# Kernel optimization log

Measured on AMD Instinct MI355X. Metric: run time of the kernel, lower is better.

The kernel has to match this reference:

```python
import jax, jax.numpy as jnp
import numpy as np

C_IN = 192
HEADS = 6
QKV_DIM = C_IN // HEADS  # 32
WH = WW = 4              # window_size
PAD_H = WH // 2          # 2
PAD_W = WW // 2          # 2


def setup_inputs() -> dict:
    key = jax.random.key(0)
    ks = jax.random.split(key, 6)
    s = 0.02
    return {
        "x": jax.random.normal(ks[0], (8, C_IN, 128, 128), jnp.float32),
        "w_qkv1": jax.random.normal(ks[1], (3 * C_IN, C_IN), jnp.float32) * s,
        "b_qkv1": jnp.zeros((3 * C_IN,), jnp.float32),
        "w_qkv2": jax.random.normal(ks[2], (3 * C_IN, C_IN), jnp.float32) * s,
        "b_qkv2": jnp.zeros((3 * C_IN,), jnp.float32),
        "w_head": jax.random.normal(ks[3], (C_IN, 2 * C_IN), jnp.float32) * s,  # 1x1 conv as matmul
        "b_head": jnp.zeros((C_IN,), jnp.float32),
    }


def _window_partition(x):
    # bchw_to_bnc: [B,C,H,W] -> [B*nh*nw, WH*WW, C]
    B, C, H, W = x.shape
    nh, nw = H // WH, W // WW
    x = x.reshape(B, C, nh, WH, nw, WW)
    x = x.transpose(0, 2, 4, 3, 5, 1)  # B,nh,nw,WH,WW,C
    return x.reshape(B * nh * nw, WH * WW, C)


def _window_merge(x, out_shape):
    # bnc_to_bchw: inverse of _window_partition
    B, C, H, W = out_shape
    nh, nw = H // WH, W // WW
    x = x.reshape(B, nh, nw, WH, WW, C)
    x = x.transpose(0, 5, 1, 3, 2, 4)  # B,C,nh,WH,nw,WW
    return x.reshape(B, C, H, W)


def _mha(xw, w, b):
    # xw: [Bn, N=16, C]; fused QKV projection then per-window SDPA
    Bn, N, C = xw.shape
    qkv = xw @ w.T + b
    q, k, v = jnp.split(qkv, 3, axis=-1)
    to_heads = lambda t: t.reshape(Bn, N, HEADS, QKV_DIM).transpose(0, 2, 1, 3)
    q, k, v = to_heads(q), to_heads(k), to_heads(v)
    scale = 1.0 / np.sqrt(QKV_DIM).astype(np.float32)
    attn = jax.nn.softmax(jnp.einsum('bhnd,bhmd->bhnm', q, k) * scale, axis=-1)
    o = jnp.einsum('bhnm,bhmd->bhnd', attn, v)
    return o.transpose(0, 2, 1, 3).reshape(Bn, N, C)


def reference(x, w_qkv1, b_qkv1, w_qkv2, b_qkv2, w_head, b_head):
    # branch 2: zero-pad by window//2 on each side (shifted windows)
    x2 = jnp.pad(x, ((0, 0), (0, 0), (PAD_H, PAD_H), (PAD_W, PAD_W)))
    s1, s2 = x.shape, x2.shape
    o1 = _window_merge(_mha(_window_partition(x), w_qkv1, b_qkv1), s1)
    o2 = _window_merge(_mha(_window_partition(x2), w_qkv2, b_qkv2), s2)
    o2 = o2[:, :, PAD_H:-PAD_H, PAD_W:-PAD_W]  # negative pad = crop
    o = jnp.concatenate([o1, o2], axis=1)      # [B, 2C, H, W]
    # 1x1 conv head projection
    return jnp.einsum('bchw,oc->bohw', o, w_head) + b_head[None, :, None, None]
```

## Files before the change

### kernel.cpp

```cpp
#include <hip/hip_runtime.h>


typedef unsigned short u16;
using bf16x8 = __attribute__((ext_vector_type(8))) short;
using f32x4  = __attribute__((ext_vector_type(4))) float;
using u16x8  = __attribute__((ext_vector_type(8))) unsigned short;
using u16x4  = __attribute__((ext_vector_type(4))) unsigned short;

#define CIN   192
#define CQKV  576
#define NW2   33

__device__ __forceinline__ float bf2f(u16 u) {
    unsigned int x = ((unsigned int)u) << 16;
    float f; __builtin_memcpy(&f, &x, 4); return f;
}
__device__ __forceinline__ u16 f2bf(float f) {
    unsigned int x; __builtin_memcpy(&x, &f, 4);
    return (u16)((x + 0x7FFFu + ((x >> 16) & 1u)) >> 16);
}
__device__ __forceinline__ int xcol(int c, int tok) {
    int blk = (c >> 3) ^ ((tok ^ (tok >> 4)) & 7);
    return blk * 8 + (c & 7);
}

__global__ void prep_conv(const float* __restrict__ w1, const float* __restrict__ w2,
                          const float* __restrict__ wh,
                          u16* __restrict__ w1b, u16* __restrict__ w2b, u16* __restrict__ whb) {
    int i = blockIdx.x * 256 + threadIdx.x;
    if (i < 110592)        w1b[i] = f2bf(w1[i]);
    else if (i < 221184)   w2b[i - 110592] = f2bf(w2[i - 110592]);
    else                   whb[i - 221184] = f2bf(wh[i - 221184]);
}

template<int BR>
__global__ __launch_bounds__(256, 2) void qkv_attn(const float* __restrict__ x,
                                                   const u16* __restrict__ wb,
                                                   const float* __restrict__ bias,
                                                   u16* __restrict__ ocat) {
    __shared__ __align__(16) char smem[77824];
    u16* xl = (u16*)smem;
    u16* wl = (u16*)(smem + 25600);
    u16* qk = (u16*)smem;
    u16* vt = (u16*)(smem + 50176);
    u16* pl = (u16*)(smem + 74752);

    const int tid  = threadIdx.x;
    const int wave = tid >> 6, lane = tid & 63;
    const int lo16 = lane & 15, quad = lane >> 4;

    int b, wy, g;
    if (BR == 0) {
        int bi = blockIdx.x;
        b = bi >> 8; int rem = bi & 255;
        wy = rem >> 3; g = rem & 7;
    } else {
        int bi = blockIdx.x;
        b = bi / 297; int rem = bi % 297;
        wy = rem / 9; g = rem % 9;
    }
    const int hbase = wy * 4, wbase = g * 16;

#pragma unroll
    for (int it = 0; it < 12; ++it) {
        int i = it * 256 + tid;
        int c = i >> 4, y = (i >> 2) & 3, xc = i & 3;
        float e0, e1, e2, e3;
        if (BR == 0) {
            const float4 v = *reinterpret_cast<const float4*>(
                &x[(((size_t)b * CIN + c) * 128 + hbase + y) * 128 + wbase + xc * 4]);
            e0 = v.x; e1 = v.y; e2 = v.z; e3 = v.w;
        } else {
            int h = hbase + y - 2;
            int w0 = wbase + xc * 4 - 2;
            bool hok = (unsigned)h < 128u;
            const float* row = &x[(((size_t)b * CIN + c) * 128 + h) * 128];
            if (hok && w0 >= 0 && w0 + 3 < 128) {
                float2 p0 = *reinterpret_cast<const float2*>(&row[w0]);
                float2 p1 = *reinterpret_cast<const float2*>(&row[w0 + 2]);
                e0 = p0.x; e1 = p0.y; e2 = p1.x; e3 = p1.y;
            } else {
                e0 = (hok && w0 >= 0 && w0 < 128)         ? row[w0]     : 0.f;
                e1 = (hok && w0+1 >= 0 && w0+1 < 128)     ? row[w0 + 1] : 0.f;
                e2 = (hok && w0+2 >= 0 && w0+2 < 128)     ? row[w0 + 2] : 0.f;
                e3 = (hok && w0+3 >= 0 && w0+3 < 128)     ? row[w0 + 3] : 0.f;
            }
        }
        int t0 = xc * 16 + y * 4;
        xl[(t0 + 0) * 200 + xcol(c, t0 + 0)] = f2bf(e0);
        xl[(t0 + 1) * 200 + xcol(c, t0 + 1)] = f2bf(e1);
        xl[(t0 + 2) * 200 + xcol(c, t0 + 2)] = f2bf(e2);
        xl[(t0 + 3) * 200 + xcol(c, t0 + 3)] = f2bf(e3);
    }
    __syncthreads();

    f32x4 acc[9][4];
#pragma unroll
    for (int mt = 0; mt < 9; ++mt)
#pragma unroll
        for (int nt = 0; nt < 4; ++nt) acc[mt][nt] = f32x4{0.f, 0.f, 0.f, 0.f};

    for (int s = 0; s < 6; ++s) {
#pragma unroll
        for (int it = 0; it < 9; ++it) {
            int i = it * 256 + tid;
            int co = i >> 2, kk = (i & 3) * 8;
            u16x8 v = *reinterpret_cast<const u16x8*>(&wb[co * 192 + s * 32 + kk]);
            *reinterpret_cast<u16x8*>(&wl[co * 40 + kk]) = v;
        }
        __syncthreads();
        bf16x8 bfr[4];
#pragma unroll
        for (int nt = 0; nt < 4; ++nt) {
            int tok = nt * 16 + lo16;
            int kb = s * 4 + quad;
            bfr[nt] = *reinterpret_cast<const bf16x8*>(
                &xl[tok * 200 + (((kb ^ ((tok ^ (tok >> 4)) & 7)) << 3))]);
        }
#pragma unroll
        for (int mt = 0; mt < 9; ++mt) {
            bf16x8 afr = *reinterpret_cast<const bf16x8*>(
                &wl[(wave * 144 + mt * 16 + lo16) * 40 + quad * 8]);
#pragma unroll
            for (int nt = 0; nt < 4; ++nt)
                acc[mt][nt] = __builtin_amdgcn_mfma_f32_16x16x32_bf16(afr, bfr[nt], acc[mt][nt], 0, 0, 0);
        }
        __syncthreads();
    }

    const float scale = 0.17677669529663687f;
#pragma unroll
    for (int mt = 0; mt < 9; ++mt) {
        int co0 = wave * 144 + mt * 16 + quad * 4;
        const float4 bv = *reinterpret_cast<const float4*>(&bias[co0]);
#pragma unroll
        for (int nt = 0; nt < 4; ++nt) {
            int tok = nt * 16 + lo16;
            float v0 = acc[mt][nt][0] + bv.x, v1 = acc[mt][nt][1] + bv.y;
            float v2 = acc[mt][nt][2] + bv.z, v3 = acc[mt][nt][3] + bv.w;
            if (co0 < 192) { v0 *= scale; v1 *= scale; v2 *= scale; v3 *= scale; }
            if (co0 < 384) {
                u16x4 pk = {f2bf(v0), f2bf(v1), f2bf(v2), f2bf(v3)};
                *reinterpret_cast<u16x4*>(&qk[tok * 392 + co0]) = pk;
            } else {
                int dh = co0 - 384;
                int head = dh >> 5, d0 = dh & 31;
                int win = tok >> 4, m = tok & 15;
                u16* vrow = &vt[((win * 6 + head) * 32 + d0) * 16 + m];
                vrow[0]  = f2bf(v0);
                vrow[16] = f2bf(v1);
                vrow[32] = f2bf(v2);
                vrow[48] = f2bf(v3);
            }
        }
    }
    __syncthreads();

    {
        const int win = wave;
        const u16* qbase = qk + (size_t)(win * 16) * 392;
        const bf16x8 z8 = {};
        const f32x4 zc = {0.f, 0.f, 0.f, 0.f};
        bool dov; size_t dst = 0;
        if (BR == 0) {
            int wg = wy * 32 + g * 4 + win;
            dst = (((size_t)(b * 1024 + wg)) * 16 + lo16) * 384;
            dov = true;
        } else {
            int wx = g * 4 + win;
            int h = wy * 4 + (lo16 >> 2) - 2;
            int w = wx * 4 + (lo16 & 3) - 2;
            dov = (wx < NW2) && (unsigned)h < 128u && (unsigned)w < 128u;
            if (dov) {
                int wg = (h >> 2) * 32 + (w >> 2);
                int nn = (h & 3) * 4 + (w & 3);
                dst = (((size_t)(b * 1024 + wg)) * 16 + nn) * 384 + 192;
            }
        }
#pragma unroll
        for (int head = 0; head < 6; ++head) {
            bf16x8 kfr = *reinterpret_cast<const bf16x8*>(
                &qbase[lo16 * 392 + 192 + head * 32 + quad * 8]);
            bf16x8 qfr = *reinterpret_cast<const bf16x8*>(
                &qbase[lo16 * 392 + head * 32 + quad * 8]);
            f32x4 st = __builtin_amdgcn_mfma_f32_16x16x32_bf16(kfr, qfr, zc, 0, 0, 0);
            float mx = fmaxf(fmaxf(st[0], st[1]), fmaxf(st[2], st[3]));
            mx = fmaxf(mx, __shfl_xor(mx, 16));
            mx = fmaxf(mx, __shfl_xor(mx, 32));
            float p0 = __expf(st[0] - mx), p1 = __expf(st[1] - mx);
            float p2 = __expf(st[2] - mx), p3 = __expf(st[3] - mx);
            float sum = p0 + p1 + p2 + p3;
            sum += __shfl_xor(sum, 16);
            sum += __shfl_xor(sum, 32);
            float inv = 1.0f / sum;
            u16x4 pk = {f2bf(p0), f2bf(p1), f2bf(p2), f2bf(p3)};
            *reinterpret_cast<u16x4*>(&pl[(wave * 16 + lo16) * 24 + quad * 4]) = pk;
            bf16x8 pf = (quad < 2)
                ? *reinterpret_cast<const bf16x8*>(&pl[(wave * 16 + lo16) * 24 + quad * 8]) : z8;
            const u16* vbase = &vt[(win * 6 + head) * 32 * 16];
#pragma unroll
            for (int half = 0; half < 2; ++half) {
                bf16x8 av = (quad < 2)
                    ? *reinterpret_cast<const bf16x8*>(&vbase[(half * 16 + lo16) * 16 + quad * 8]) : z8;
                f32x4 o = __builtin_amdgcn_mfma_f32_16x16x32_bf16(av, pf, zc, 0, 0, 0);
                if (dov) {
                    u16x4 ok = {f2bf(o[0] * inv), f2bf(o[1] * inv),
                                f2bf(o[2] * inv), f2bf(o[3] * inv)};
                    *reinterpret_cast<u16x4*>(&ocat[dst + head * 32 + half * 16 + quad * 4]) = ok;
                }
            }
        }
    }
}

__global__ __launch_bounds__(256, 3) void head_gemm(const u16* __restrict__ ocat,
                                                    const u16* __restrict__ whb,
                                                    const float* __restrict__ bh,
                                                    float* __restrict__ out) {
    __shared__ __align__(16) u16 bt[64 * 392];
    const int tid = threadIdx.x;
    const int wave = tid >> 6, lane = tid & 63;
    const int lo16 = lane & 15, quad = lane >> 4;

    int bi = blockIdx.x;
    int b = bi >> 8; int rem = bi & 255;
    int wy = rem >> 3, g = rem & 7;
    const int wg0 = wy * 32 + g * 4;
    const size_t gbase = ((size_t)(b * 1024 + wg0) * 16) * 384;

#pragma unroll
    for (int it = 0; it < 12; ++it) {
        int i = it * 256 + tid;
        u16x8 v = *reinterpret_cast<const u16x8*>(&ocat[gbase + (size_t)i * 8]);
        int row = i / 48, kc = i - row * 48;
        *reinterpret_cast<u16x8*>(&bt[row * 392 + kc * 8]) = v;
    }
    __syncthreads();

    const int co_base = wave * 48;
    f32x4 acc[3][4];
#pragma unroll
    for (int mt = 0; mt < 3; ++mt)
#pragma unroll
        for (int nt = 0; nt < 4; ++nt) acc[mt][nt] = f32x4{0.f, 0.f, 0.f, 0.f};

#pragma unroll
    for (int s = 0; s < 12; ++s) {
        int k0 = s * 32;
        bf16x8 a[3], bb[4];
#pragma unroll
        for (int nt = 0; nt < 4; ++nt)
            bb[nt] = *reinterpret_cast<const bf16x8*>(&bt[(nt * 16 + lo16) * 392 + k0 + quad * 8]);
#pragma unroll
        for (int mt = 0; mt < 3; ++mt)
            a[mt] = *reinterpret_cast<const bf16x8*>(
                &whb[(size_t)(co_base + mt * 16 + lo16) * 384 + k0 + quad * 8]);
#pragma unroll
        for (int mt = 0; mt < 3; ++mt)
#pragma unroll
            for (int nt = 0; nt < 4; ++nt)
                acc[mt][nt] = __builtin_amdgcn_mfma_f32_16x16x32_bf16(a[mt], bb[nt], acc[mt][nt], 0, 0, 0);
    }

    int h = wy * 4 + (lo16 >> 2);
#pragma unroll
    for (int mt = 0; mt < 3; ++mt) {
        int co0 = co_base + mt * 16 + quad * 4;
        const float4 bv = *reinterpret_cast<const float4*>(&bh[co0]);
#pragma unroll
        for (int r = 0; r < 4; ++r) {
            float bias = (r == 0) ? bv.x : (r == 1) ? bv.y : (r == 2) ? bv.z : bv.w;
#pragma unroll
            for (int nt = 0; nt < 4; ++nt) {
                int w = (g * 4 + nt) * 4 + (lo16 & 3);
                out[(((size_t)b * CIN + co0 + r) * 128 + h) * 128 + w] = acc[mt][nt][r] + bias;
            }
        }
    }
}

extern "C" void kernel_launch(void* const* d_in, const int* in_sizes, int n_in,
                              void* d_out, int out_size, void* d_ws, size_t ws_size,
                              hipStream_t stream) {
    const float* x  = (const float*)d_in[0];
    const float* w1 = (const float*)d_in[1];
    const float* b1 = (const float*)d_in[2];
    const float* w2 = (const float*)d_in[3];
    const float* b2 = (const float*)d_in[4];
    const float* wh = (const float*)d_in[5];
    const float* bh = (const float*)d_in[6];
    float* out = (float*)d_out;

    char* ws = (char*)d_ws;
    u16* ocat = (u16*)ws;
    u16* w1b  = (u16*)(ws + 100663296);
    u16* w2b  = (u16*)(ws + 100884480);
    u16* whb  = (u16*)(ws + 101105664);

    prep_conv<<<1152, 256, 0, stream>>>(w1, w2, wh, w1b, w2b, whb);
    qkv_attn<0><<<2048, 256, 0, stream>>>(x, w1b, b1, ocat);
    qkv_attn<1><<<2376, 256, 0, stream>>>(x, w2b, b2, ocat);
    head_gemm<<<2048, 256, 0, stream>>>(ocat, whb, bh, out);
}
```

Baseline: 455.5 us.

## Merge both attention branches into one launch and read weights straight from global

The two templated branch kernels become a single launch of 4424 blocks. A swizzled block index interleaves branch-0 and branch-1 blocks across XCDs, and each block picks its weights, bias and load path at runtime. The per-K-step weight staging into LDS and its two barriers are removed; each wave now loads its A fragments directly from global or L2. This cuts barrier stalls and the kernel-launch gap, but adds uncoalesced-ish global loads in the MFMA loop, possibly higher latency, and runtime branching where the branch used to be a compile-time template.

```diff
diff --git a/kernel.cpp b/kernel.cpp
--- a/kernel.cpp
+++ b/kernel.cpp
@@ -33,14 +33,14 @@
     else                   whb[i - 221184] = f2bf(wh[i - 221184]);
 }
 
-template<int BR>
 __global__ __launch_bounds__(256, 2) void qkv_attn(const float* __restrict__ x,
-                                                   const u16* __restrict__ wb,
-                                                   const float* __restrict__ bias,
+                                                   const u16* __restrict__ w1b,
+                                                   const float* __restrict__ b1,
+                                                   const u16* __restrict__ w2b,
+                                                   const float* __restrict__ b2,
                                                    u16* __restrict__ ocat) {
     __shared__ __align__(16) char smem[77824];
     u16* xl = (u16*)smem;
-    u16* wl = (u16*)(smem + 25600);
     u16* qk = (u16*)smem;
     u16* vt = (u16*)(smem + 50176);
     u16* pl = (u16*)(smem + 74752);
@@ -49,28 +49,42 @@
     const int wave = tid >> 6, lane = tid & 63;
     const int lo16 = lane & 15, quad = lane >> 4;
 
+    const int swz = (blockIdx.x & 7) * 553 + (blockIdx.x >> 3);
+    const bool br0 = (swz < 2048);
+
     int b, wy, g;
-    if (BR == 0) {
-        int bi = blockIdx.x;
-        b = bi >> 8; int rem = bi & 255;
+    const u16* wb; const float* bias;
+    if (br0) {
+        b = swz >> 8; int rem = swz & 255;
         wy = rem >> 3; g = rem & 7;
+        wb = w1b; bias = b1;
     } else {
-        int bi = blockIdx.x;
+        int bi = swz - 2048;
         b = bi / 297; int rem = bi % 297;
         wy = rem / 9; g = rem % 9;
+        wb = w2b; bias = b2;
     }
     const int hbase = wy * 4, wbase = g * 16;
 
-#pragma unroll
-    for (int it = 0; it < 12; ++it) {
-        int i = it * 256 + tid;
-        int c = i >> 4, y = (i >> 2) & 3, xc = i & 3;
-        float e0, e1, e2, e3;
-        if (BR == 0) {
+    if (br0) {
+#pragma unroll
+        for (int it = 0; it < 12; ++it) {
+            int i = it * 256 + tid;
+            int c = i >> 4, y = (i >> 2) & 3, xc = i & 3;
             const float4 v = *reinterpret_cast<const float4*>(
                 &x[(((size_t)b * CIN + c) * 128 + hbase + y) * 128 + wbase + xc * 4]);
-            e0 = v.x; e1 = v.y; e2 = v.z; e3 = v.w;
-        } else {
+            int t0 = xc * 16 + y * 4;
+            xl[(t0 + 0) * 200 + xcol(c, t0 + 0)] = f2bf(v.x);
+            xl[(t0 + 1) * 200 + xcol(c, t0 + 1)] = f2bf(v.y);
+            xl[(t0 + 2) * 200 + xcol(c, t0 + 2)] = f2bf(v.z);
+            xl[(t0 + 3) * 200 + xcol(c, t0 + 3)] = f2bf(v.w);
+        }
+    } else {
+#pragma unroll
+        for (int it = 0; it < 12; ++it) {
+            int i = it * 256 + tid;
+            int c = i >> 4, y = (i >> 2) & 3, xc = i & 3;
+            float e0, e1, e2, e3;
             int h = hbase + y - 2;
             int w0 = wbase + xc * 4 - 2;
             bool hok = (unsigned)h < 128u;
@@ -85,12 +99,12 @@
                 e2 = (hok && w0+2 >= 0 && w0+2 < 128)     ? row[w0 + 2] : 0.f;
                 e3 = (hok && w0+3 >= 0 && w0+3 < 128)     ? row[w0 + 3] : 0.f;
             }
-        }
-        int t0 = xc * 16 + y * 4;
-        xl[(t0 + 0) * 200 + xcol(c, t0 + 0)] = f2bf(e0);
-        xl[(t0 + 1) * 200 + xcol(c, t0 + 1)] = f2bf(e1);
-        xl[(t0 + 2) * 200 + xcol(c, t0 + 2)] = f2bf(e2);
-        xl[(t0 + 3) * 200 + xcol(c, t0 + 3)] = f2bf(e3);
+            int t0 = xc * 16 + y * 4;
+            xl[(t0 + 0) * 200 + xcol(c, t0 + 0)] = f2bf(e0);
+            xl[(t0 + 1) * 200 + xcol(c, t0 + 1)] = f2bf(e1);
+            xl[(t0 + 2) * 200 + xcol(c, t0 + 2)] = f2bf(e2);
+            xl[(t0 + 3) * 200 + xcol(c, t0 + 3)] = f2bf(e3);
+        }
     }
     __syncthreads();
 
@@ -100,15 +114,9 @@
 #pragma unroll
         for (int nt = 0; nt < 4; ++nt) acc[mt][nt] = f32x4{0.f, 0.f, 0.f, 0.f};
 
+    const u16* wrow = wb + (size_t)(wave * 144 + lo16) * 192 + quad * 8;
+#pragma unroll
     for (int s = 0; s < 6; ++s) {
-#pragma unroll
-        for (int it = 0; it < 9; ++it) {
-            int i = it * 256 + tid;
-            int co = i >> 2, kk = (i & 3) * 8;
-            u16x8 v = *reinterpret_cast<const u16x8*>(&wb[co * 192 + s * 32 + kk]);
-            *reinterpret_cast<u16x8*>(&wl[co * 40 + kk]) = v;
-        }
-        __syncthreads();
         bf16x8 bfr[4];
 #pragma unroll
         for (int nt = 0; nt < 4; ++nt) {
@@ -119,14 +127,13 @@
         }
 #pragma unroll
         for (int mt = 0; mt < 9; ++mt) {
-            bf16x8 afr = *reinterpret_cast<const bf16x8*>(
-                &wl[(wave * 144 + mt * 16 + lo16) * 40 + quad * 8]);
+            bf16x8 afr = *reinterpret_cast<const bf16x8*>(&wrow[mt * 3072 + s * 32]);
 #pragma unroll
             for (int nt = 0; nt < 4; ++nt)
                 acc[mt][nt] = __builtin_amdgcn_mfma_f32_16x16x32_bf16(afr, bfr[nt], acc[mt][nt], 0, 0, 0);
         }
-        __syncthreads();
-    }
+    }
+    __syncthreads();
 
     const float scale = 0.17677669529663687f;
 #pragma unroll
@@ -162,7 +169,7 @@
         const bf16x8 z8 = {};
         const f32x4 zc = {0.f, 0.f, 0.f, 0.f};
         bool dov; size_t dst = 0;
-        if (BR == 0) {
+        if (br0) {
             int wg = wy * 32 + g * 4 + win;
             dst = (((size_t)(b * 1024 + wg)) * 16 + lo16) * 384;
             dov = true;
@@ -298,7 +305,6 @@
     u16* whb  = (u16*)(ws + 101105664);
 
     prep_conv<<<1152, 256, 0, stream>>>(w1, w2, wh, w1b, w2b, whb);
-    qkv_attn<0><<<2048, 256, 0, stream>>>(x, w1b, b1, ocat);
-    qkv_attn<1><<<2376, 256, 0, stream>>>(x, w2b, b2, ocat);
+    qkv_attn<<<4424, 256, 0, stream>>>(x, w1b, b1, w2b, b2, ocat);
     head_gemm<<<2048, 256, 0, stream>>>(ocat, whb, bh, out);
 }
```

New measurement: 485.4 us. 6.6% more time.
